# Optimization experiments

Measured on AMD Instinct MI355X. Metric: run time of the kernel, lower is better.

Reference implementation:

```python
import jax, jax.numpy as jnp
import numpy as np

T, N, ENC_DIM, DEC_DIM, ATTN_DIM = 2048, 64, 1024, 1024, 256


def setup_inputs() -> dict:
    key = jax.random.key(0)
    k1, k2, k3, k4, k5 = jax.random.split(key, 5)
    enc_out = jax.random.normal(k1, (T, N, ENC_DIM), dtype=jnp.float32)
    dec_h = jax.random.normal(k2, (N, DEC_DIM), dtype=jnp.float32)
    # Linear weights stored as [out, in] like torch; scaled like default init
    W_e = jax.random.normal(k3, (ATTN_DIM, ENC_DIM), dtype=jnp.float32) / np.sqrt(ENC_DIM)
    W_d = jax.random.normal(k4, (ATTN_DIM, DEC_DIM), dtype=jnp.float32) / np.sqrt(DEC_DIM)
    v = jax.random.normal(k5, (1, ATTN_DIM), dtype=jnp.float32) / np.sqrt(ATTN_DIM)
    return {"enc_out": enc_out, "dec_h": dec_h, "W_e": W_e, "W_d": W_d, "v": v}


def reference(enc_out, dec_h, W_e, W_d, v):
    # e_proj: [T, N, A]; d_proj: [1, N, A]
    e_proj = jnp.einsum('tne,ae->tna', enc_out, W_e)
    d_proj = jnp.einsum('nd,ad->na', dec_h, W_d)[None, :, :]
    # scores: [T, N] = tanh(e+d) @ v
    scores = jnp.einsum('tna,a->tn', jnp.tanh(e_proj + d_proj), v[0])
    alpha = jax.nn.softmax(scores, axis=0)  # softmax over time dim
    ctx = jnp.einsum('tn,tne->ne', alpha, enc_out)  # [N, E]
    return (ctx, alpha)
```

## Files before the change

### kernel.cpp

```cpp
#include <hip/hip_runtime.h>
#include <math.h>

#define T_DIM 2048
#define N_DIM 64
#define E_DIM 1024
#define A_DIM 256
#define TCHUNK 32
#define NCHUNK (T_DIM / TCHUNK)

typedef __bf16 bf16x8 __attribute__((ext_vector_type(8)));
typedef __bf16 bf16x4 __attribute__((ext_vector_type(4)));
typedef float f32x4 __attribute__((ext_vector_type(4)));

__device__ __forceinline__ float tanh_fast(float x) {
    float xc = fminf(fmaxf(x, -15.f), 15.f);
    float e = __expf(2.f * xc);
    return (e - 1.f) / (e + 1.f);
}

__global__ __launch_bounds__(256) void convert_W(const float* __restrict__ W_e,
                                                 __bf16* __restrict__ Wp) {
    const int uid = blockIdx.x * 256 + threadIdx.x;
    const int a = uid >> 7;
    const int c = uid & 127;
    const float4* src = (const float4*)(W_e + (size_t)a * E_DIM + c * 8);
    float4 x0 = src[0], x1 = src[1];
    bf16x8 o;
    o[0] = (__bf16)x0.x; o[1] = (__bf16)x0.y; o[2] = (__bf16)x0.z; o[3] = (__bf16)x0.w;
    o[4] = (__bf16)x1.x; o[5] = (__bf16)x1.y; o[6] = (__bf16)x1.z; o[7] = (__bf16)x1.w;
    *(bf16x8*)(Wp + ((size_t)c * 256 + a) * 8) = o;
}

__global__ __launch_bounds__(256) void dproj_kernel(
    const float* __restrict__ dec_h, const float* __restrict__ W_d,
    float* __restrict__ d_proj) {
    __shared__ float dec[E_DIM];
    const int n = blockIdx.x;
    const int tid = threadIdx.x;
    reinterpret_cast<float4*>(dec)[tid] =
        reinterpret_cast<const float4*>(dec_h + (size_t)n * E_DIM)[tid];
    __syncthreads();
    const float* w = W_d + (size_t)tid * E_DIM;
    float acc = 0.f;
#pragma unroll 4
    for (int e = 0; e < E_DIM; e += 4) {
        float4 wv = *reinterpret_cast<const float4*>(w + e);
        acc = fmaf(wv.x, dec[e], acc);
        acc = fmaf(wv.y, dec[e + 1], acc);
        acc = fmaf(wv.z, dec[e + 2], acc);
        acc = fmaf(wv.w, dec[e + 3], acc);
    }
    d_proj[n * A_DIM + tid] = acc;
}

__global__ __launch_bounds__(256, 2) void flash_kernel(
    const float* __restrict__ enc, const __bf16* __restrict__ Wp,
    const float* __restrict__ dproj, const float* __restrict__ v,
    float* __restrict__ scores, float* __restrict__ partial,
    float* __restrict__ ms, float* __restrict__ zs) {
    __shared__ __align__(16) __bf16 Atile[TCHUNK * E_DIM];
    float* red = ((float*)Atile) + 16384 - 160;
    float* wls = red + 128;

    const int tid = threadIdx.x;
    const int bid = blockIdx.x;
    const int n = bid & (N_DIM - 1);
    const int c = bid >> 6;
    const int t0 = c * TCHUNK;
    const int wn = tid >> 6, lane = tid & 63;
    const int lr = lane & 15, lg = lane >> 4;

    f32x4 acc[2][4];
#pragma unroll
    for (int i = 0; i < 2; ++i)
#pragma unroll
        for (int j = 0; j < 4; ++j) acc[i][j] = (f32x4){0.f, 0.f, 0.f, 0.f};

    float vv[4], dp[4];
#pragma unroll
    for (int fn = 0; fn < 4; ++fn) {
        const int a = wn * 64 + fn * 16 + lr;
        vv[fn] = v[a];
        dp[fn] = dproj[n * A_DIM + a];
    }

    const int srow = tid >> 3, sg8 = tid & 7;
    const int sg = sg8 >> 1, shalf = sg8 & 1;
    const float* encRow =
        enc + ((size_t)(t0 + srow) * N_DIM + n) * E_DIM + sg8 * 4;
    const bf16x8* WpV = (const bf16x8*)Wp;

    float4 c0a = *(const float4*)(encRow);
    float4 c0b = *(const float4*)(encRow + 32);

    for (int kt = 0; kt < 16; ++kt) {
        bf16x8 bfr[8];
        const int ks0 = kt * 2;
#pragma unroll
        for (int s = 0; s < 2; ++s)
#pragma unroll
            for (int fn = 0; fn < 4; ++fn)
                bfr[s * 4 + fn] = WpV[(size_t)(ks0 + s) * 1024 + lg * 256 +
                                      wn * 64 + fn * 16 + lr];
        float4 na, nb;
        if (kt < 15) {
            const float* p = encRow + (kt + 1) * 64;
            na = *(const float4*)p;
            nb = *(const float4*)(p + 32);
        }
        {
            bf16x4 w0, w1;
            w0[0] = (__bf16)c0a.x; w0[1] = (__bf16)c0a.y;
            w0[2] = (__bf16)c0a.z; w0[3] = (__bf16)c0a.w;
            w1[0] = (__bf16)c0b.x; w1[1] = (__bf16)c0b.y;
            w1[2] = (__bf16)c0b.z; w1[3] = (__bf16)c0b.w;
            const int u0 = ks0 * 128 + sg * 32 + (srow ^ ((ks0 * 4 + sg) & 7));
            const int u1 = (ks0 + 1) * 128 + sg * 32 +
                           (srow ^ (((ks0 + 1) * 4 + sg) & 7));
            *(bf16x4*)((char*)Atile + u0 * 16 + shalf * 8) = w0;
            *(bf16x4*)((char*)Atile + u1 * 16 + shalf * 8) = w1;
        }
        __syncthreads();
#pragma unroll
        for (int s = 0; s < 2; ++s) {
            const int ks = ks0 + s;
#pragma unroll
            for (int fm = 0; fm < 2; ++fm) {
                const int row = fm * 16 + lr;
                const int u =
                    ks * 128 + lg * 32 + (row ^ ((ks * 4 + lg) & 7));
                bf16x8 af = *(const bf16x8*)((const char*)Atile + u * 16);
                acc[fm][0] = __builtin_amdgcn_mfma_f32_16x16x32_bf16(af, bfr[s*4+0], acc[fm][0], 0, 0, 0);
                acc[fm][1] = __builtin_amdgcn_mfma_f32_16x16x32_bf16(af, bfr[s*4+1], acc[fm][1], 0, 0, 0);
                acc[fm][2] = __builtin_amdgcn_mfma_f32_16x16x32_bf16(af, bfr[s*4+2], acc[fm][2], 0, 0, 0);
                acc[fm][3] = __builtin_amdgcn_mfma_f32_16x16x32_bf16(af, bfr[s*4+3], acc[fm][3], 0, 0, 0);
            }
        }
        c0a = na;
        c0b = nb;
    }

    float pr[2][4];
#pragma unroll
    for (int fm = 0; fm < 2; ++fm) {
#pragma unroll
        for (int reg = 0; reg < 4; ++reg) {
            float p = 0.f;
#pragma unroll
            for (int fn = 0; fn < 4; ++fn)
                p = fmaf(vv[fn], tanh_fast(acc[fm][fn][reg] + dp[fn]), p);
            p += __shfl_xor(p, 1);
            p += __shfl_xor(p, 2);
            p += __shfl_xor(p, 4);
            p += __shfl_xor(p, 8);
            pr[fm][reg] = p;
        }
    }
    __syncthreads();
    if (lr == 0) {
#pragma unroll
        for (int fm = 0; fm < 2; ++fm)
#pragma unroll
            for (int reg = 0; reg < 4; ++reg)
                red[wn * 32 + fm * 16 + lg * 4 + reg] = pr[fm][reg];
    }
    __syncthreads();
    if (tid < TCHUNK) {
        float s = red[tid] + red[32 + tid] + red[64 + tid] + red[96 + tid];
        scores[(t0 + tid) * N_DIM + n] = s;
        if (partial) {
            float m = s;
            m = fmaxf(m, __shfl_xor(m, 1));
            m = fmaxf(m, __shfl_xor(m, 2));
            m = fmaxf(m, __shfl_xor(m, 4));
            m = fmaxf(m, __shfl_xor(m, 8));
            m = fmaxf(m, __shfl_xor(m, 16));
            float w = __expf(s - m);
            float Z = w;
            Z += __shfl_xor(Z, 1);
            Z += __shfl_xor(Z, 2);
            Z += __shfl_xor(Z, 4);
            Z += __shfl_xor(Z, 8);
            Z += __shfl_xor(Z, 16);
            wls[tid] = w;
            if (tid == 0) {
                ms[n * NCHUNK + c] = m;
                zs[n * NCHUNK + c] = Z;
            }
        }
    }
    __syncthreads();

    if (!partial) return;
    f32x4 a4 = (f32x4){0.f, 0.f, 0.f, 0.f};
    if (tid < 252) {
        const int ks = tid >> 3, g = (tid >> 1) & 3, half = tid & 1;
        const int q = (ks * 4 + g) & 7;
        const int ubase = ks * 128 + g * 32;
#pragma unroll 4
        for (int r = 0; r < TCHUNK; ++r) {
            const float w = wls[r];
            bf16x4 ev = *(const bf16x4*)((const char*)Atile +
                                         (ubase + (r ^ q)) * 16 + half * 8);
            a4[0] = fmaf(w, (float)ev[0], a4[0]);
            a4[1] = fmaf(w, (float)ev[1], a4[1]);
            a4[2] = fmaf(w, (float)ev[2], a4[2]);
            a4[3] = fmaf(w, (float)ev[3], a4[3]);
        }
    } else {
#pragma unroll 4
        for (int r = 0; r < TCHUNK; ++r) {
            const float w = wls[r];
            float4 ev = *(const float4*)(
                enc + ((size_t)(t0 + r) * N_DIM + n) * E_DIM + tid * 4);
            a4[0] = fmaf(w, ev.x, a4[0]);
            a4[1] = fmaf(w, ev.y, a4[1]);
            a4[2] = fmaf(w, ev.z, a4[2]);
            a4[3] = fmaf(w, ev.w, a4[3]);
        }
    }
    *(f32x4*)(partial + ((size_t)c * N_DIM + n) * E_DIM + tid * 4) = a4;
}

__global__ __launch_bounds__(256) void combine_kernel(
    const float* __restrict__ partial, const float* __restrict__ ms,
    const float* __restrict__ zs, const float* __restrict__ scores,
    float* __restrict__ ctx, float* __restrict__ alpha) {
    __shared__ float scale[NCHUNK];
    __shared__ float MZ[2];
    const int n = blockIdx.x;
    const int tid = threadIdx.x;
    if (tid < NCHUNK) {
        float m = ms[n * NCHUNK + tid];
        float M = m;
        M = fmaxf(M, __shfl_xor(M, 1));
        M = fmaxf(M, __shfl_xor(M, 2));
        M = fmaxf(M, __shfl_xor(M, 4));
        M = fmaxf(M, __shfl_xor(M, 8));
        M = fmaxf(M, __shfl_xor(M, 16));
        M = fmaxf(M, __shfl_xor(M, 32));
        float e = __expf(m - M);
        float z = zs[n * NCHUNK + tid] * e;
        float Z = z;
        Z += __shfl_xor(Z, 1);
        Z += __shfl_xor(Z, 2);
        Z += __shfl_xor(Z, 4);
        Z += __shfl_xor(Z, 8);
        Z += __shfl_xor(Z, 16);
        Z += __shfl_xor(Z, 32);
        scale[tid] = e;
        if (tid == 0) {
            MZ[0] = M;
            MZ[1] = Z;
        }
    }
    __syncthreads();
    const float M = MZ[0];
    const float invZ = 1.f / MZ[1];
    f32x4 a4 = (f32x4){0.f, 0.f, 0.f, 0.f};
    for (int c = 0; c < NCHUNK; ++c) {
        const float s = scale[c] * invZ;
        float4 p = *(const float4*)(partial +
                                    ((size_t)c * N_DIM + n) * E_DIM + tid * 4);
        a4[0] = fmaf(s, p.x, a4[0]);
        a4[1] = fmaf(s, p.y, a4[1]);
        a4[2] = fmaf(s, p.z, a4[2]);
        a4[3] = fmaf(s, p.w, a4[3]);
    }
    *(f32x4*)(ctx + (size_t)n * E_DIM + tid * 4) = a4;
    for (int t = tid; t < T_DIM; t += 256)
        alpha[t * N_DIM + n] = __expf(scores[t * N_DIM + n] - M) * invZ;
}

__global__ __launch_bounds__(256) void softmax_kernel(
    const float* __restrict__ scores, float* __restrict__ alpha) {
    __shared__ float red[256];
    const int n = blockIdx.x;
    const int tid = threadIdx.x;
    float m = -3.4e38f;
    for (int t = tid; t < T_DIM; t += 256)
        m = fmaxf(m, scores[t * N_DIM + n]);
    red[tid] = m;
    __syncthreads();
    for (int s = 128; s; s >>= 1) {
        if (tid < s) red[tid] = fmaxf(red[tid], red[tid + s]);
        __syncthreads();
    }
    m = red[0];
    __syncthreads();
    float sum = 0.f;
    for (int t = tid; t < T_DIM; t += 256)
        sum += expf(scores[t * N_DIM + n] - m);
    red[tid] = sum;
    __syncthreads();
    for (int s = 128; s; s >>= 1) {
        if (tid < s) red[tid] += red[tid + s];
        __syncthreads();
    }
    const float inv = 1.f / red[0];
    for (int t = tid; t < T_DIM; t += 256)
        alpha[t * N_DIM + n] = expf(scores[t * N_DIM + n] - m) * inv;
}

__global__ __launch_bounds__(256) void ctx_f32(const float* __restrict__ enc,
                                               const float* __restrict__ alpha,
                                               float* __restrict__ ctx) {
    const int n = blockIdx.x;
    const int tid = threadIdx.x;
    float4 acc = {0.f, 0.f, 0.f, 0.f};
    for (int t = 0; t < T_DIM; ++t) {
        const float al = alpha[t * N_DIM + n];
        float4 ev = *reinterpret_cast<const float4*>(
            enc + (size_t)(t * N_DIM + n) * E_DIM + tid * 4);
        acc.x = fmaf(al, ev.x, acc.x);
        acc.y = fmaf(al, ev.y, acc.y);
        acc.z = fmaf(al, ev.z, acc.z);
        acc.w = fmaf(al, ev.w, acc.w);
    }
    *reinterpret_cast<float4*>(ctx + (size_t)n * E_DIM + tid * 4) = acc;
}

extern "C" void kernel_launch(void* const* d_in, const int* in_sizes, int n_in,
                              void* d_out, int out_size, void* d_ws,
                              size_t ws_size, hipStream_t stream) {
    const float* enc = (const float*)d_in[0];
    const float* dec_h = (const float*)d_in[1];
    const float* W_e = (const float*)d_in[2];
    const float* W_d = (const float*)d_in[3];
    const float* v = (const float*)d_in[4];

    float* out = (float*)d_out;
    float* ctx = out;
    float* alpha = out + 65536;

    float* ws = (float*)d_ws;
    float* d_proj = ws;
    float* scores = ws + 16384;
    __bf16* Wp = (__bf16*)(ws + 147456);
    float* ms = ws + 278528;
    float* zs = ws + 282624;
    float* partial = ws + 286720;

    const size_t need = (size_t)(286720 + NCHUNK * N_DIM * E_DIM) * sizeof(float);
    const bool big = ws_size >= need;

    convert_W<<<128, 256, 0, stream>>>(W_e, Wp);
    dproj_kernel<<<N_DIM, 256, 0, stream>>>(dec_h, W_d, d_proj);
    flash_kernel<<<T_DIM / TCHUNK * N_DIM, 256, 0, stream>>>(
        enc, Wp, d_proj, v, scores, big ? partial : nullptr, ms, zs);
    if (big) {
        combine_kernel<<<N_DIM, 256, 0, stream>>>(partial, ms, zs, scores,
                                                  ctx, alpha);
    } else {
        softmax_kernel<<<N_DIM, 256, 0, stream>>>(scores, alpha);
        ctx_f32<<<N_DIM, 256, 0, stream>>>(enc, alpha, ctx);
    }
}
```

Measured before the change: 264.0 us.

## Double flash kernel threads to 512, splitting attention columns across 8 waves

The flash kernel now runs 512 threads (8 waves) per block, each wave owning 32 attention columns instead of 64. Each loop iteration covers 4 k-steps instead of 2, so there are fewer barriers, and the enc staging is split across 16 threads per row. The context partial sum now splits the 32 time rows between thread pairs and combines them with a shuffle. The aim is more parallelism and latency hiding per block for this memory-bound workload, at the cost of more reduction steps and possible register or LDS occupancy pressure.

```diff
diff --git a/kernel.cpp b/kernel.cpp
--- a/kernel.cpp
+++ b/kernel.cpp
@@ -53,87 +53,88 @@
     d_proj[n * A_DIM + tid] = acc;
 }
 
-__global__ __launch_bounds__(256, 2) void flash_kernel(
+__global__ __launch_bounds__(512, 4) void flash_kernel(
     const float* __restrict__ enc, const __bf16* __restrict__ Wp,
     const float* __restrict__ dproj, const float* __restrict__ v,
     float* __restrict__ scores, float* __restrict__ partial,
     float* __restrict__ ms, float* __restrict__ zs) {
     __shared__ __align__(16) __bf16 Atile[TCHUNK * E_DIM];
-    float* red = ((float*)Atile) + 16384 - 160;
-    float* wls = red + 128;
+    float* red = ((float*)Atile) + 16384 - 288;
+    float* wls = red + 256;
 
     const int tid = threadIdx.x;
     const int bid = blockIdx.x;
     const int n = bid & (N_DIM - 1);
     const int c = bid >> 6;
     const int t0 = c * TCHUNK;
-    const int wn = tid >> 6, lane = tid & 63;
+    const int wn = tid >> 6;
+    const int lane = tid & 63;
     const int lr = lane & 15, lg = lane >> 4;
 
-    f32x4 acc[2][4];
+    f32x4 acc[2][2];
 #pragma unroll
     for (int i = 0; i < 2; ++i)
 #pragma unroll
-        for (int j = 0; j < 4; ++j) acc[i][j] = (f32x4){0.f, 0.f, 0.f, 0.f};
-
-    float vv[4], dp[4];
-#pragma unroll
-    for (int fn = 0; fn < 4; ++fn) {
-        const int a = wn * 64 + fn * 16 + lr;
+        for (int j = 0; j < 2; ++j) acc[i][j] = (f32x4){0.f, 0.f, 0.f, 0.f};
+
+    float vv[2], dp[2];
+#pragma unroll
+    for (int fn = 0; fn < 2; ++fn) {
+        const int a = wn * 32 + fn * 16 + lr;
         vv[fn] = v[a];
         dp[fn] = dproj[n * A_DIM + a];
     }
 
-    const int srow = tid >> 3, sg8 = tid & 7;
-    const int sg = sg8 >> 1, shalf = sg8 & 1;
+    const int srow = tid >> 4, sg = tid & 15;
+    const int sgg = (sg & 7) >> 1, sbh = sg & 1;
+    const int sks = sg >> 3;
     const float* encRow =
-        enc + ((size_t)(t0 + srow) * N_DIM + n) * E_DIM + sg8 * 4;
+        enc + ((size_t)(t0 + srow) * N_DIM + n) * E_DIM + sg * 4;
     const bf16x8* WpV = (const bf16x8*)Wp;
 
-    float4 c0a = *(const float4*)(encRow);
-    float4 c0b = *(const float4*)(encRow + 32);
-
-    for (int kt = 0; kt < 16; ++kt) {
-        bf16x8 bfr[8];
-        const int ks0 = kt * 2;
-#pragma unroll
-        for (int s = 0; s < 2; ++s)
-#pragma unroll
-            for (int fn = 0; fn < 4; ++fn)
-                bfr[s * 4 + fn] = WpV[(size_t)(ks0 + s) * 1024 + lg * 256 +
-                                      wn * 64 + fn * 16 + lr];
-        float4 na, nb;
-        if (kt < 15) {
-            const float* p = encRow + (kt + 1) * 64;
-            na = *(const float4*)p;
-            nb = *(const float4*)(p + 32);
-        }
+    float4 c0a = *(const float4*)encRow;
+    float4 c0b = *(const float4*)(encRow + 64);
+
+#pragma unroll 1
+    for (int it = 0; it < 8; ++it) {
         {
+            const int ks1 = it * 4 + sks, ks2 = ks1 + 2;
             bf16x4 w0, w1;
             w0[0] = (__bf16)c0a.x; w0[1] = (__bf16)c0a.y;
             w0[2] = (__bf16)c0a.z; w0[3] = (__bf16)c0a.w;
             w1[0] = (__bf16)c0b.x; w1[1] = (__bf16)c0b.y;
             w1[2] = (__bf16)c0b.z; w1[3] = (__bf16)c0b.w;
-            const int u0 = ks0 * 128 + sg * 32 + (srow ^ ((ks0 * 4 + sg) & 7));
-            const int u1 = (ks0 + 1) * 128 + sg * 32 +
-                           (srow ^ (((ks0 + 1) * 4 + sg) & 7));
-            *(bf16x4*)((char*)Atile + u0 * 16 + shalf * 8) = w0;
-            *(bf16x4*)((char*)Atile + u1 * 16 + shalf * 8) = w1;
+            const int u1 = ks1 * 128 + sgg * 32 + (srow ^ ((ks1 * 4 + sgg) & 7));
+            const int u2 = ks2 * 128 + sgg * 32 + (srow ^ ((ks2 * 4 + sgg) & 7));
+            *(bf16x4*)((char*)Atile + u1 * 16 + sbh * 8) = w0;
+            *(bf16x4*)((char*)Atile + u2 * 16 + sbh * 8) = w1;
+        }
+        bf16x8 bfr[4][2];
+#pragma unroll
+        for (int s = 0; s < 4; ++s)
+#pragma unroll
+            for (int fn = 0; fn < 2; ++fn)
+                bfr[s][fn] = WpV[(size_t)(it * 4 + s) * 1024 + lg * 256 +
+                                 wn * 32 + fn * 16 + lr];
+        float4 na, nb;
+        if (it < 7) {
+            const float* p = encRow + (it + 1) * 128;
+            na = *(const float4*)p;
+            nb = *(const float4*)(p + 64);
         }
         __syncthreads();
 #pragma unroll
-        for (int s = 0; s < 2; ++s) {
-            const int ks = ks0 + s;
+        for (int s = 0; s < 4; ++s) {
+            const int ks = it * 4 + s;
 #pragma unroll
             for (int fm = 0; fm < 2; ++fm) {
-                const int row = fm * 16 + lr;
                 const int u =
-                    ks * 128 + lg * 32 + (row ^ ((ks * 4 + lg) & 7));
+                    ks * 128 + lg * 32 + ((fm * 16 + lr) ^ ((ks * 4 + lg) & 7));
                 bf16x8 af = *(const bf16x8*)((const char*)Atile + u * 16);
-                acc[fm][0] = __builtin_amdgcn_mfma_f32_16x16x32_bf16(af, bfr[s*4+0], acc[fm][0], 0, 0, 0);
-                acc[fm][1] = __builtin_amdgcn_mfma_f32_16x16x32_bf16(af, bfr[s*4+1], acc[fm][1], 0, 0, 0);
-                acc[fm][2] = __builtin_amdgcn_mfma_f32_16x16x32_bf16(af, bfr[s*4+2], acc[fm][2], 0, 0, 0);
-                acc[fm][3] = __builtin_amdgcn_mfma_f32_16x16x32_bf16(af, bfr[s*4+3], acc[fm][3], 0, 0, 0);
+                acc[fm][0] = __builtin_amdgcn_mfma_f32_16x16x32_bf16(
+                    af, bfr[s][0], acc[fm][0], 0, 0, 0);
+                acc[fm][1] = __builtin_amdgcn_mfma_f32_16x16x32_bf16(
+                    af, bfr[s][1], acc[fm][1], 0, 0, 0);
             }
         }
         c0a = na;
@@ -145,10 +146,8 @@
     for (int fm = 0; fm < 2; ++fm) {
 #pragma unroll
         for (int reg = 0; reg < 4; ++reg) {
-            float p = 0.f;
-#pragma unroll
-            for (int fn = 0; fn < 4; ++fn)
-                p = fmaf(vv[fn], tanh_fast(acc[fm][fn][reg] + dp[fn]), p);
+            float p = fmaf(vv[0], tanh_fast(acc[fm][0][reg] + dp[0]), 0.f);
+            p = fmaf(vv[1], tanh_fast(acc[fm][1][reg] + dp[1]), p);
             p += __shfl_xor(p, 1);
             p += __shfl_xor(p, 2);
             p += __shfl_xor(p, 4);
@@ -166,7 +165,9 @@
     }
     __syncthreads();
     if (tid < TCHUNK) {
-        float s = red[tid] + red[32 + tid] + red[64 + tid] + red[96 + tid];
+        float s = 0.f;
+#pragma unroll
+        for (int w = 0; w < 8; ++w) s += red[w * 32 + tid];
         scores[(t0 + tid) * N_DIM + n] = s;
         if (partial) {
             float m = s;
@@ -192,16 +193,18 @@
     __syncthreads();
 
     if (!partial) return;
+    const int cs = tid >> 1, rh = tid & 1;
+    const int ks = cs >> 3, gg = (cs >> 1) & 3, bh = cs & 1;
+    const int colbase = ks * 32 + gg * 8 + bh * 4;
     f32x4 a4 = (f32x4){0.f, 0.f, 0.f, 0.f};
-    if (tid < 252) {
-        const int ks = tid >> 3, g = (tid >> 1) & 3, half = tid & 1;
-        const int q = (ks * 4 + g) & 7;
-        const int ubase = ks * 128 + g * 32;
+    if (cs < 250) {
+        const int q = (ks * 4 + gg) & 7;
+        const int ubase = ks * 128 + gg * 32;
 #pragma unroll 4
-        for (int r = 0; r < TCHUNK; ++r) {
+        for (int r = rh * 16; r < rh * 16 + 16; ++r) {
             const float w = wls[r];
             bf16x4 ev = *(const bf16x4*)((const char*)Atile +
-                                         (ubase + (r ^ q)) * 16 + half * 8);
+                                         (ubase + (r ^ q)) * 16 + bh * 8);
             a4[0] = fmaf(w, (float)ev[0], a4[0]);
             a4[1] = fmaf(w, (float)ev[1], a4[1]);
             a4[2] = fmaf(w, (float)ev[2], a4[2]);
@@ -209,17 +212,20 @@
         }
     } else {
 #pragma unroll 4
-        for (int r = 0; r < TCHUNK; ++r) {
+        for (int r = rh * 16; r < rh * 16 + 16; ++r) {
             const float w = wls[r];
             float4 ev = *(const float4*)(
-                enc + ((size_t)(t0 + r) * N_DIM + n) * E_DIM + tid * 4);
+                enc + ((size_t)(t0 + r) * N_DIM + n) * E_DIM + colbase);
             a4[0] = fmaf(w, ev.x, a4[0]);
             a4[1] = fmaf(w, ev.y, a4[1]);
             a4[2] = fmaf(w, ev.z, a4[2]);
             a4[3] = fmaf(w, ev.w, a4[3]);
         }
     }
-    *(f32x4*)(partial + ((size_t)c * N_DIM + n) * E_DIM + tid * 4) = a4;
+#pragma unroll
+    for (int k = 0; k < 4; ++k) a4[k] += __shfl_xor(a4[k], 1);
+    if (rh == 0)
+        *(f32x4*)(partial + ((size_t)c * N_DIM + n) * E_DIM + colbase) = a4;
 }
 
 __global__ __launch_bounds__(256) void combine_kernel(
@@ -258,6 +264,7 @@
     const float M = MZ[0];
     const float invZ = 1.f / MZ[1];
     f32x4 a4 = (f32x4){0.f, 0.f, 0.f, 0.f};
+#pragma unroll 4
     for (int c = 0; c < NCHUNK; ++c) {
         const float s = scale[c] * invZ;
         float4 p = *(const float4*)(partial +
@@ -341,12 +348,13 @@
     float* zs = ws + 282624;
     float* partial = ws + 286720;
 
-    const size_t need = (size_t)(286720 + NCHUNK * N_DIM * E_DIM) * sizeof(float);
+    const size_t need =
+        (size_t)(286720 + NCHUNK * N_DIM * E_DIM) * sizeof(float);
     const bool big = ws_size >= need;
 
     convert_W<<<128, 256, 0, stream>>>(W_e, Wp);
     dproj_kernel<<<N_DIM, 256, 0, stream>>>(dec_h, W_d, d_proj);
-    flash_kernel<<<T_DIM / TCHUNK * N_DIM, 256, 0, stream>>>(
+    flash_kernel<<<T_DIM / TCHUNK * N_DIM, 512, 0, stream>>>(
         enc, Wp, d_proj, v, scores, big ? partial : nullptr, ms, zs);
     if (big) {
         combine_kernel<<<N_DIM, 256, 0, stream>>>(partial, ms, zs, scores,
```

After: 232.9 us. 11.8% less time.
